# Optimization experiments

Measured on AMD Instinct MI355X. Metric: run time of the kernel, lower is better.

Reference implementation:

```python
import jax, jax.numpy as jnp
import numpy as np

NUM_LABELS = 80
GROUPS = 512
OUT_PER_GROUP = 4  # 2048 / 512
K = 14  # kernel == spatial size -> 1x1 output


def setup_inputs() -> dict:
    key = jax.random.key(0)
    ks = jax.random.split(key, 8)
    B = 256
    x = jax.random.normal(ks[0], (B, NUM_LABELS, K, K), dtype=jnp.float32)
    # conv1: 1x1, num_labels -> 512 (store as [out,in])
    w1 = jax.random.normal(ks[1], (512, NUM_LABELS), dtype=jnp.float32) * 0.05
    b1 = jax.random.normal(ks[2], (512,), dtype=jnp.float32) * 0.01
    # conv2: 1x1, 512 -> 512
    w2 = jax.random.normal(ks[3], (512, 512), dtype=jnp.float32) * 0.05
    b2 = jax.random.normal(ks[4], (512,), dtype=jnp.float32) * 0.01
    # conv3 (grouped): per group, 1 in-ch -> 4 out-ch, 14x14 kernel, no bias
    w3 = jax.random.normal(ks[5], (GROUPS, OUT_PER_GROUP, K, K), dtype=jnp.float32) * 0.02
    # fc: 2048 -> num_labels (torch Linear layout [out,in])
    fc_w = jax.random.normal(ks[6], (NUM_LABELS, GROUPS * OUT_PER_GROUP), dtype=jnp.float32) * 0.02
    fc_b = jax.random.normal(ks[7], (NUM_LABELS,), dtype=jnp.float32) * 0.01
    return {"x": x, "w1": w1, "b1": b1, "w2": w2, "b2": b2,
            "w3": w3, "fc_w": fc_w, "fc_b": fc_b}


def reference(x, w1, b1, w2, b2, w3, fc_w, fc_b):
    # conv1: 1x1 conv == channel GEMM. x: [B,C,H,W]
    h = jnp.einsum('bchw,oc->bohw', x, w1) + b1[None, :, None, None]
    # conv2: 1x1 conv, 512 -> 512
    h = jnp.einsum('bchw,oc->bohw', h, w2) + b2[None, :, None, None]
    # conv3: 512 independent group convs (1 in-ch each, full 14x14 kernel,
    # no padding) -> output spatial 1x1. Fused into a single contraction.
    # h: [B, G, H, W], w3: [G, O, H, W] -> [B, G, O]
    g = jnp.einsum('bghw,gohw->bgo', h, w3)
    g = jax.nn.relu(g)
    # torch.cat over groups then flatten == reshape [B, G*O]
    flat = g.reshape(g.shape[0], GROUPS * OUT_PER_GROUP)
    return flat @ fc_w.T + fc_b
```

## Files before the change

### kernel.cpp

```cpp
#include <hip/hip_runtime.h>
#include <hip/hip_bf16.h>

#define CIN 80
#define NSP 196
#define HWP 208
#define KP  96

#define NBA 4096
#define NBB 1024
#define NBC 512
#define NBD 64
#define NBE 16

typedef __attribute__((ext_vector_type(8))) short  short8;
typedef __attribute__((ext_vector_type(4))) float  floatx4;
typedef __attribute__((ext_vector_type(4))) unsigned short ushort4v;

static __device__ __forceinline__ unsigned short f2b(float f) {
    __hip_bfloat16 h = __float2bfloat16(f);
    return *(unsigned short*)&h;
}
static __device__ __forceinline__ float b2f(unsigned short u) {
    unsigned int x = ((unsigned int)u) << 16;
    float f; __builtin_memcpy(&f, &x, 4); return f;
}

__global__ __launch_bounds__(384) void kPre(
    const float* __restrict__ x,  const float* __restrict__ w1,
    const float* __restrict__ b1, const float* __restrict__ w2,
    const float* __restrict__ b2, const float* __restrict__ w3,
    const float* __restrict__ fc_w, const float* __restrict__ fc_b,
    float* __restrict__ Wcf, unsigned short* __restrict__ xbf,
    unsigned short* __restrict__ w3tb, unsigned short* __restrict__ fctb,
    float* __restrict__ out)
{
    __shared__ float tile[80 * 53];
    const int blk = blockIdx.x, t = threadIdx.x;

    if (blk < NBA) {
        const int o4 = blk >> 5, kc = blk & 31;
        const int lc = t % 96, oi = t / 96;
        const int o = o4 * 4 + oi;
        const int m0 = kc * 16;
        if (lc <= CIN) {
            const float* __restrict__ w2p = w2 + (size_t)o * 512 + m0;
            float part = 0.f;
            if (lc < CIN) {
                const float* __restrict__ w1p = w1 + (size_t)m0 * CIN + lc;
                #pragma unroll
                for (int i = 0; i < 16; ++i)
                    part = fmaf(w2p[i], w1p[(size_t)i * CIN], part);
            } else {
                #pragma unroll
                for (int i = 0; i < 16; ++i)
                    part = fmaf(w2p[i], b1[m0 + i], part);
                if (kc == 31) part += b2[o];
            }
            atomicAdd(Wcf + o * KP + lc, part);
        }
    } else if (blk < NBA + NBB) {
        const int r = blk - NBA;
        const int b = r >> 2, qt = r & 3, hw0 = qt * 52;
        for (int idx = t; idx < 80 * 52; idx += 384) {
            const int k = idx / 52, hl = idx - k * 52;
            const int hw = hw0 + hl;
            tile[k * 53 + hl] = (hw < NSP) ? x[(size_t)b * CIN * NSP + k * NSP + hw] : 0.f;
        }
        __syncthreads();
        unsigned short* __restrict__ ob = xbf + (size_t)b * HWP * KP;
        for (int idx = t; idx < 52 * 24; idx += 384) {
            const int hl = idx / 24, kq = idx - hl * 24;
            const int hw = hw0 + hl;
            ushort4v v;
            #pragma unroll
            for (int j = 0; j < 4; ++j) {
                const int k = kq * 4 + j;
                float f = 0.f;
                if (hw < NSP) {
                    if (k < CIN) f = tile[k * 53 + hl];
                    else if (k == CIN) f = 1.f;
                }
                v[j] = f2b(f);
            }
            *(ushort4v*)(ob + (size_t)hw * KP + kq * 4) = v;
        }
    } else if (blk < NBA + NBB + NBC) {
        const int g = blk - NBA - NBB;
        if (t < HWP) {
            ushort4v v;
            #pragma unroll
            for (int o = 0; o < 4; ++o)
                v[o] = f2b((t < NSP) ? w3[(size_t)g * 4 * NSP + o * NSP + t] : 0.f);
            *(ushort4v*)(w3tb + ((size_t)g * HWP + t) * 4) = v;
        }
    } else if (blk < NBA + NBB + NBC + NBD) {
        const int base = (blk - NBA - NBB - NBC) * 2560;
        for (int i = t; i < 2560; i += 384) {
            const int idx = base + i;
            const int k = idx / CIN, l = idx - k * CIN;
            fctb[idx] = f2b(fc_w[(size_t)l * 2048 + k]);
        }
    } else {
        const int base = (blk - NBA - NBB - NBC - NBD) * 1280;
        for (int i = t; i < 1280; i += 384) {
            const int idx = base + i;
            out[idx] = fc_b[idx - (idx / CIN) * CIN];
        }
    }
}

__global__ __launch_bounds__(256) void kM(
    const unsigned short* __restrict__ xbf, const float* __restrict__ Wcf,
    const unsigned short* __restrict__ w3tb, const unsigned short* __restrict__ fctb,
    float* __restrict__ out)
{
    __shared__ float gl[2 * 256];
    const int bp = blockIdx.x, gc = blockIdx.y;
    const int t = threadIdx.x;
    const int w = t >> 6, lane = t & 63;
    const int col = lane & 15, quad = lane >> 4;
    const int g0 = gc * 64 + w * 16;
    const int b0 = bp * 2;

    short8 A[3];
    {
        const float* __restrict__ ap = Wcf + (size_t)(g0 + col) * KP + quad * 8;
        #pragma unroll
        for (int ks = 0; ks < 3; ++ks) {
            const floatx4 lo = *(const floatx4*)(ap + ks * 32);
            const floatx4 hi = *(const floatx4*)(ap + ks * 32 + 4);
            short8 s;
            #pragma unroll
            for (int j = 0; j < 4; ++j) {
                s[j]     = (short)f2b(lo[j]);
                s[4 + j] = (short)f2b(hi[j]);
            }
            A[ks] = s;
        }
    }

    float p[2][4][4];
    #pragma unroll
    for (int bi = 0; bi < 2; ++bi)
        #pragma unroll
        for (int r = 0; r < 4; ++r)
            #pragma unroll
            for (int o = 0; o < 4; ++o) p[bi][r][o] = 0.f;

    const unsigned short* __restrict__ xb =
        xbf + ((size_t)b0 * HWP + col) * KP + quad * 8;
    const unsigned short* __restrict__ wb =
        w3tb + ((size_t)(g0 + quad * 4) * HWP + col) * 4;

    #pragma unroll 1
    for (int nt = 0; nt < 13; ++nt) {
        float wv[4][4];
        #pragma unroll
        for (int r = 0; r < 4; ++r) {
            const ushort4v u = *(const ushort4v*)(wb + ((size_t)r * HWP + nt * 16) * 4);
            wv[r][0] = b2f(u[0]); wv[r][1] = b2f(u[1]);
            wv[r][2] = b2f(u[2]); wv[r][3] = b2f(u[3]);
        }
        #pragma unroll
        for (int bi = 0; bi < 2; ++bi) {
            const unsigned short* __restrict__ xp = xb + ((size_t)bi * HWP + nt * 16) * KP;
            const short8 x0 = *(const short8*)(xp);
            const short8 x1 = *(const short8*)(xp + 32);
            const short8 x2 = *(const short8*)(xp + 64);
            floatx4 acc = {0.f, 0.f, 0.f, 0.f};
            acc = __builtin_amdgcn_mfma_f32_16x16x32_bf16(A[0], x0, acc, 0, 0, 0);
            acc = __builtin_amdgcn_mfma_f32_16x16x32_bf16(A[1], x1, acc, 0, 0, 0);
            acc = __builtin_amdgcn_mfma_f32_16x16x32_bf16(A[2], x2, acc, 0, 0, 0);
            #pragma unroll
            for (int r = 0; r < 4; ++r) {
                p[bi][r][0] = fmaf(acc[r], wv[r][0], p[bi][r][0]);
                p[bi][r][1] = fmaf(acc[r], wv[r][1], p[bi][r][1]);
                p[bi][r][2] = fmaf(acc[r], wv[r][2], p[bi][r][2]);
                p[bi][r][3] = fmaf(acc[r], wv[r][3], p[bi][r][3]);
            }
        }
    }

    #pragma unroll
    for (int bi = 0; bi < 2; ++bi)
        #pragma unroll
        for (int r = 0; r < 4; ++r) {
            float q0 = p[bi][r][0], q1 = p[bi][r][1], q2 = p[bi][r][2], q3 = p[bi][r][3];
            #pragma unroll
            for (int s = 8; s >= 1; s >>= 1) {
                q0 += __shfl_down(q0, s, 16);
                q1 += __shfl_down(q1, s, 16);
                q2 += __shfl_down(q2, s, 16);
                q3 += __shfl_down(q3, s, 16);
            }
            if (col == 0) {
                const int glocal = w * 16 + quad * 4 + r;
                floatx4 ov = {fmaxf(q0, 0.f), fmaxf(q1, 0.f), fmaxf(q2, 0.f), fmaxf(q3, 0.f)};
                *(floatx4*)(gl + bi * 256 + glocal * 4) = ov;
            }
        }
    __syncthreads();

    if (t < 160) {
        const int l = t % CIN, half = t / CIN;
        const unsigned short* __restrict__ fr =
            fctb + (size_t)(gc * 256 + half * 128) * CIN + l;
        const float* __restrict__ gp = gl + half * 128;
        float s0 = 0.f, s1 = 0.f;
        #pragma unroll 4
        for (int kk = 0; kk < 128; ++kk) {
            const float fv = b2f(fr[(size_t)kk * CIN]);
            s0 = fmaf(gp[kk      ], fv, s0);
            s1 = fmaf(gp[kk + 256], fv, s1);
        }
        atomicAdd(out + (b0 + 0) * CIN + l, s0);
        atomicAdd(out + (b0 + 1) * CIN + l, s1);
    }
}

extern "C" void kernel_launch(void* const* d_in, const int* in_sizes, int n_in,
                              void* d_out, int out_size, void* d_ws, size_t ws_size,
                              hipStream_t stream) {
    const float* x    = (const float*)d_in[0];
    const float* w1   = (const float*)d_in[1];
    const float* b1   = (const float*)d_in[2];
    const float* w2   = (const float*)d_in[3];
    const float* b2   = (const float*)d_in[4];
    const float* w3   = (const float*)d_in[5];
    const float* fc_w = (const float*)d_in[6];
    const float* fc_b = (const float*)d_in[7];
    float* out = (float*)d_out;

    const int B = in_sizes[0] / (CIN * NSP);

    char* ws = (char*)d_ws;
    unsigned short* xbf = (unsigned short*)ws;
    size_t off = (size_t)B * HWP * KP * 2;
    float* Wcf = (float*)(ws + off);                   off += 512 * KP * 4;
    unsigned short* w3tb = (unsigned short*)(ws + off); off += (size_t)512 * HWP * 4 * 2;
    unsigned short* fctb = (unsigned short*)(ws + off);

    hipMemsetAsync(Wcf, 0, 512 * KP * 4, stream);
    kPre<<<NBA + NBB + NBC + NBD + NBE, 384, 0, stream>>>(
        x, w1, b1, w2, b2, w3, fc_w, fc_b, Wcf, xbf, w3tb, fctb, out);
    kM<<<dim3(B / 2, 8), 256, 0, stream>>>(xbf, Wcf, w3tb, fctb, out);
}
```

Measured before the change: 133.0 us.

## Stage per-batch activations in LDS and remap blocks to one batch, 128 groups

The main kernel now gives each block one batch element and 128 groups (512 threads) instead of two batch elements and 64 groups. The block copies that batch's bf16 activation tile into padded shared memory once, and all eight waves read MFMA operands from there instead of from global memory. The per-position w3 weights are prefetched one iteration ahead into registers. This cuts redundant global reads of x across group-chunk blocks (8 to 4) and hides weight load latency, but it adds about 43KB of LDS per block, which may limit occupancy, and it drops the reuse of weights across two batch elements.

Measured after the change: 139.4 us. +4.8%, slower.

```diff
diff --git a/kernel.cpp b/kernel.cpp
--- a/kernel.cpp
+++ b/kernel.cpp
@@ -5,6 +5,7 @@
 #define NSP 196
 #define HWP 208
 #define KP  96
+#define XST 104
 
 #define NBA 4096
 #define NBB 1024
@@ -109,18 +110,27 @@
     }
 }
 
-__global__ __launch_bounds__(256) void kM(
+__global__ __launch_bounds__(512) void kM(
     const unsigned short* __restrict__ xbf, const float* __restrict__ Wcf,
     const unsigned short* __restrict__ w3tb, const unsigned short* __restrict__ fctb,
     float* __restrict__ out)
 {
-    __shared__ float gl[2 * 256];
-    const int bp = blockIdx.x, gc = blockIdx.y;
+    __shared__ __align__(16) unsigned short xs[HWP * XST];
+    __shared__ float gl[512];
+    const int b = blockIdx.x, gc = blockIdx.y;
     const int t = threadIdx.x;
+
+    {
+        const ushort4v* __restrict__ src = (const ushort4v*)(xbf + (size_t)b * HWP * KP);
+        for (int idx = t; idx < HWP * 24; idx += 512) {
+            const int r = idx / 24, c = idx - r * 24;
+            *(ushort4v*)(xs + r * XST + c * 4) = src[r * 24 + c];
+        }
+    }
+
     const int w = t >> 6, lane = t & 63;
     const int col = lane & 15, quad = lane >> 4;
-    const int g0 = gc * 64 + w * 16;
-    const int b0 = bp * 2;
+    const int g0 = gc * 128 + w * 16;
 
     short8 A[3];
     {
@@ -139,82 +149,79 @@
         }
     }
 
-    float p[2][4][4];
+    float p[4][4];
     #pragma unroll
-    for (int bi = 0; bi < 2; ++bi)
-        #pragma unroll
-        for (int r = 0; r < 4; ++r)
-            #pragma unroll
-            for (int o = 0; o < 4; ++o) p[bi][r][o] = 0.f;
-
-    const unsigned short* __restrict__ xb =
-        xbf + ((size_t)b0 * HWP + col) * KP + quad * 8;
+    for (int r = 0; r < 4; ++r)
+        #pragma unroll
+        for (int o = 0; o < 4; ++o) p[r][o] = 0.f;
+
     const unsigned short* __restrict__ wb =
         w3tb + ((size_t)(g0 + quad * 4) * HWP + col) * 4;
+    const unsigned short* __restrict__ xrow = xs + col * XST + quad * 8;
+
+    __syncthreads();
+
+    ushort4v cw[4];
+    #pragma unroll
+    for (int r = 0; r < 4; ++r)
+        cw[r] = *(const ushort4v*)(wb + (size_t)r * HWP * 4);
 
     #pragma unroll 1
     for (int nt = 0; nt < 13; ++nt) {
-        float wv[4][4];
+        const int ntn = (nt < 12) ? nt + 1 : 12;
+        ushort4v nw[4];
+        #pragma unroll
+        for (int r = 0; r < 4; ++r)
+            nw[r] = *(const ushort4v*)(wb + ((size_t)r * HWP + ntn * 16) * 4);
+
+        const unsigned short* __restrict__ xp = xrow + nt * 16 * XST;
+        const short8 x0 = *(const short8*)(xp);
+        const short8 x1 = *(const short8*)(xp + 32);
+        const short8 x2 = *(const short8*)(xp + 64);
+        floatx4 acc = {0.f, 0.f, 0.f, 0.f};
+        acc = __builtin_amdgcn_mfma_f32_16x16x32_bf16(A[0], x0, acc, 0, 0, 0);
+        acc = __builtin_amdgcn_mfma_f32_16x16x32_bf16(A[1], x1, acc, 0, 0, 0);
+        acc = __builtin_amdgcn_mfma_f32_16x16x32_bf16(A[2], x2, acc, 0, 0, 0);
+
         #pragma unroll
         for (int r = 0; r < 4; ++r) {
-            const ushort4v u = *(const ushort4v*)(wb + ((size_t)r * HWP + nt * 16) * 4);
-            wv[r][0] = b2f(u[0]); wv[r][1] = b2f(u[1]);
-            wv[r][2] = b2f(u[2]); wv[r][3] = b2f(u[3]);
-        }
-        #pragma unroll
-        for (int bi = 0; bi < 2; ++bi) {
-            const unsigned short* __restrict__ xp = xb + ((size_t)bi * HWP + nt * 16) * KP;
-            const short8 x0 = *(const short8*)(xp);
-            const short8 x1 = *(const short8*)(xp + 32);
-            const short8 x2 = *(const short8*)(xp + 64);
-            floatx4 acc = {0.f, 0.f, 0.f, 0.f};
-            acc = __builtin_amdgcn_mfma_f32_16x16x32_bf16(A[0], x0, acc, 0, 0, 0);
-            acc = __builtin_amdgcn_mfma_f32_16x16x32_bf16(A[1], x1, acc, 0, 0, 0);
-            acc = __builtin_amdgcn_mfma_f32_16x16x32_bf16(A[2], x2, acc, 0, 0, 0);
-            #pragma unroll
-            for (int r = 0; r < 4; ++r) {
-                p[bi][r][0] = fmaf(acc[r], wv[r][0], p[bi][r][0]);
-                p[bi][r][1] = fmaf(acc[r], wv[r][1], p[bi][r][1]);
-                p[bi][r][2] = fmaf(acc[r], wv[r][2], p[bi][r][2]);
-                p[bi][r][3] = fmaf(acc[r], wv[r][3], p[bi][r][3]);
-            }
-        }
+            p[r][0] = fmaf(acc[r], b2f(cw[r][0]), p[r][0]);
+            p[r][1] = fmaf(acc[r], b2f(cw[r][1]), p[r][1]);
+            p[r][2] = fmaf(acc[r], b2f(cw[r][2]), p[r][2]);
+            p[r][3] = fmaf(acc[r], b2f(cw[r][3]), p[r][3]);
+        }
+        #pragma unroll
+        for (int r = 0; r < 4; ++r) cw[r] = nw[r];
     }
 
     #pragma unroll
-    for (int bi = 0; bi < 2; ++bi)
-        #pragma unroll
-        for (int r = 0; r < 4; ++r) {
-            float q0 = p[bi][r][0], q1 = p[bi][r][1], q2 = p[bi][r][2], q3 = p[bi][r][3];
-            #pragma unroll
-            for (int s = 8; s >= 1; s >>= 1) {
-                q0 += __shfl_down(q0, s, 16);
-                q1 += __shfl_down(q1, s, 16);
-                q2 += __shfl_down(q2, s, 16);
-                q3 += __shfl_down(q3, s, 16);
-            }
-            if (col == 0) {
-                const int glocal = w * 16 + quad * 4 + r;
-                floatx4 ov = {fmaxf(q0, 0.f), fmaxf(q1, 0.f), fmaxf(q2, 0.f), fmaxf(q3, 0.f)};
-                *(floatx4*)(gl + bi * 256 + glocal * 4) = ov;
-            }
-        }
+    for (int r = 0; r < 4; ++r) {
+        float q0 = p[r][0], q1 = p[r][1], q2 = p[r][2], q3 = p[r][3];
+        #pragma unroll
+        for (int s = 8; s >= 1; s >>= 1) {
+            q0 += __shfl_down(q0, s, 16);
+            q1 += __shfl_down(q1, s, 16);
+            q2 += __shfl_down(q2, s, 16);
+            q3 += __shfl_down(q3, s, 16);
+        }
+        if (col == 0) {
+            const int glocal = w * 16 + quad * 4 + r;
+            floatx4 ov = {fmaxf(q0, 0.f), fmaxf(q1, 0.f), fmaxf(q2, 0.f), fmaxf(q3, 0.f)};
+            *(floatx4*)(gl + glocal * 4) = ov;
+        }
+    }
     __syncthreads();
 
-    if (t < 160) {
-        const int l = t % CIN, half = t / CIN;
+    if (t < 320) {
+        const int l = t % CIN, q = t / CIN;
         const unsigned short* __restrict__ fr =
-            fctb + (size_t)(gc * 256 + half * 128) * CIN + l;
-        const float* __restrict__ gp = gl + half * 128;
-        float s0 = 0.f, s1 = 0.f;
+            fctb + (size_t)(gc * 512 + q * 128) * CIN + l;
+        const float* __restrict__ gp = gl + q * 128;
+        float s = 0.f;
         #pragma unroll 4
-        for (int kk = 0; kk < 128; ++kk) {
-            const float fv = b2f(fr[(size_t)kk * CIN]);
-            s0 = fmaf(gp[kk      ], fv, s0);
-            s1 = fmaf(gp[kk + 256], fv, s1);
-        }
-        atomicAdd(out + (b0 + 0) * CIN + l, s0);
-        atomicAdd(out + (b0 + 1) * CIN + l, s1);
+        for (int kk = 0; kk < 128; ++kk)
+            s = fmaf(gp[kk], b2f(fr[(size_t)kk * CIN]), s);
+        atomicAdd(out + b * CIN + l, s);
     }
 }
 
@@ -243,5 +250,5 @@
     hipMemsetAsync(Wcf, 0, 512 * KP * 4, stream);
     kPre<<<NBA + NBB + NBC + NBD + NBE, 384, 0, stream>>>(
         x, w1, b1, w2, b2, w3, fc_w, fc_b, Wcf, xbf, w3tb, fctb, out);
-    kM<<<dim3(B / 2, 8), 256, 0, stream>>>(xbf, Wcf, w3tb, fctb, out);
-}
+    kM<<<dim3(B, 4), 512, 0, stream>>>(xbf, Wcf, w3tb, fctb, out);
+}
```
